# Kernel tuning notes

Measured on AMD Instinct MI355X. Metric: run time of the kernel, lower is better.

The kernel has to match this reference:

```python
import jax, jax.numpy as jnp
import numpy as np

H = 16       # num query heads
KV = 4       # num kv heads
D = 64       # head_dim
EPS = 1e-6


def setup_inputs() -> dict:
    key = jax.random.key(0)
    ks = jax.random.split(key, 12)
    B, N, E = 2, 2048, 1024
    s = 0.02
    return {
        "x": jax.random.normal(ks[0], (B, N, E), jnp.float32),
        "sin": jax.random.normal(ks[1], (N, D), jnp.float32),
        "cos": jax.random.normal(ks[2], (N, D), jnp.float32),
        "wq_w": jax.random.normal(ks[3], (E, E), jnp.float32) * s,
        "wq_b": jax.random.normal(ks[4], (E,), jnp.float32) * s,
        "wk_w": jax.random.normal(ks[5], (KV * D, E), jnp.float32) * s,
        "wk_b": jax.random.normal(ks[6], (KV * D,), jnp.float32) * s,
        "wv_w": jax.random.normal(ks[7], (KV * D, E), jnp.float32) * s,
        "wv_b": jax.random.normal(ks[8], (KV * D,), jnp.float32) * s,
        "qn_w": jnp.ones((D,), jnp.float32),
        "kn_w": jnp.ones((D,), jnp.float32),
        "proj_w": jax.random.normal(ks[9], (E, E), jnp.float32) * s,
        "proj_b": jax.random.normal(ks[10], (E,), jnp.float32) * s,
    }


def _rmsnorm(t, w):
    # t: [..., D]
    var = jnp.mean(t * t, axis=-1, keepdims=True)
    return t * jax.lax.rsqrt(var + EPS) * w


def _rope(t, sin, cos):
    # t: [B,h,N,D]; sin/cos: [N,D] broadcast
    x1, x2 = jnp.split(t, 2, axis=-1)
    rotated = jnp.concatenate([-x2, x1], axis=-1)
    return t * cos + rotated * sin


def reference(x, sin, cos, wq_w, wq_b, wk_w, wk_b, wv_w, wv_b,
              qn_w, kn_w, proj_w, proj_b):
    B, N, E = x.shape
    q = (x @ wq_w.T + wq_b).reshape(B, N, H, D).transpose(0, 2, 1, 3)   # [B,H,N,D]
    k = (x @ wk_w.T + wk_b).reshape(B, N, KV, D).transpose(0, 2, 1, 3)  # [B,KV,N,D]
    v = (x @ wv_w.T + wv_b).reshape(B, N, KV, D).transpose(0, 2, 1, 3)
    q = _rmsnorm(q, qn_w)
    k = _rmsnorm(k, kn_w)
    # GQA: repeat kv heads to match query heads (repeat_interleave on head dim)
    factor = H // KV
    k = jnp.repeat(k, factor, axis=1)  # [B,H,N,D]
    v = jnp.repeat(v, factor, axis=1)
    # RoPE (n_extra = 0 since sin covers full sequence)
    q = _rope(q, sin, cos)
    k = _rope(k, sin, cos)
    # scaled dot-product attention
    scale = 1.0 / np.sqrt(D).astype(np.float32)
    scores = jnp.einsum("bhqd,bhkd->bhqk", q, k) * scale
    attn = jax.nn.softmax(scores, axis=-1)
    out = jnp.einsum("bhqk,bhkd->bhqd", attn, v)      # [B,H,N,D]
    out = out.transpose(0, 2, 1, 3).reshape(B, N, E)  # [B,N,E]
    return out @ proj_w.T + proj_b
```

## Files before the change

### kernel.cpp

```cpp
#include <hip/hip_runtime.h>
#include <hip/hip_bf16.h>
#include <math.h>


#define N_SEQ 2048
#define EMB   1024
#define NH    16
#define NKV   4
#define HD    64
#define BATCH 2
#define M_TOT 4096
#define QKV_N 1536

typedef __attribute__((ext_vector_type(8)))  short short8;
typedef __attribute__((ext_vector_type(4)))  float f32x4;
typedef __attribute__((ext_vector_type(16))) float f32x16;

__device__ __forceinline__ ushort f2bf(float f) {
    union { __hip_bfloat16 h; ushort u; } cv;
    cv.h = __float2bfloat16(f);
    return cv.u;
}
__device__ __forceinline__ float bf2f(ushort u) {
    union { __hip_bfloat16 h; ushort u; } cv;
    cv.u = u;
    return __bfloat162float(cv.h);
}
__device__ __forceinline__ uint pack2bf(float a, float b) {
    union { __hip_bfloat162 h; uint u; } cv;
    cv.h = __float22bfloat162_rn(float2{a, b});
    return cv.u;
}

__device__ __forceinline__ void g2lds16(const ushort* g, ushort* l) {
    __builtin_amdgcn_global_load_lds(
        (const __attribute__((address_space(1))) unsigned int*)g,
        (__attribute__((address_space(3))) unsigned int*)l, 16, 0, 0);
}

__device__ __forceinline__ void cvt4(const float* __restrict__ s,
                                     ushort* __restrict__ d, long g, long gd) {
    const float4 v = ((const float4*)s)[g];
    ushort4 o;
    o.x = f2bf(v.x); o.y = f2bf(v.y); o.z = f2bf(v.z); o.w = f2bf(v.w);
    ((ushort4*)d)[gd] = o;
}

__global__ __launch_bounds__(256) void prep_kernel(
    const float* __restrict__ x,  const float* __restrict__ wq,
    const float* __restrict__ wk, const float* __restrict__ wv,
    const float* __restrict__ wp, const float* __restrict__ bq,
    const float* __restrict__ bk, const float* __restrict__ bv,
    ushort* __restrict__ xb, ushort* __restrict__ Wqkv,
    ushort* __restrict__ Wproj, float* __restrict__ bqkv)
{
    const long i = (long)blockIdx.x * 256 + threadIdx.x;
    if (i < 1048576) {
        cvt4(x, xb, i, i);
    } else if (i < 1310720) {
        const long g = i - 1048576;
        cvt4(wq, Wqkv, g, g);
    } else if (i < 1376256) {
        const long g = i - 1310720;
        cvt4(wk, Wqkv, g, 262144 + g);
    } else if (i < 1441792) {
        const long g = i - 1376256;
        cvt4(wv, Wqkv, g, 327680 + g);
    } else if (i < 1703936) {
        const long g = i - 1441792;
        cvt4(wp, Wproj, g, g);
    } else if (i < 1704320) {
        const long j = i - 1703936;
        float4 v;
        if (j < 256)      v = ((const float4*)bq)[j];
        else if (j < 320) v = ((const float4*)bk)[j - 256];
        else              v = ((const float4*)bv)[j - 320];
        ((float4*)bqkv)[j] = v;
    }
}

__global__ __launch_bounds__(256) void gemm_qkv_fused(
    const ushort* __restrict__ A, const ushort* __restrict__ W,
    const float* __restrict__ bias,
    const float* __restrict__ qn_w, const float* __restrict__ kn_w,
    const float* __restrict__ sinp, const float* __restrict__ cosp,
    ushort* __restrict__ Qb, ushort* __restrict__ Kf,
    ushort* __restrict__ Vf)
{
    __shared__ ushort SMEM[6144];
    ushort* As = SMEM;
    ushort* Bs = SMEM + 4096;

    const int tid = threadIdx.x;
    const int m0 = blockIdx.y * 128, n0 = blockIdx.x * 64;
    const int w = tid >> 6, lane = tid & 63;
    const int quad = lane >> 4, l16 = lane & 15;
    const int wm = w * 32;
    const int K = EMB;

    f32x4 acc[2][4] = {};

    float bb[4];
#pragma unroll
    for (int j = 0; j < 4; ++j) bb[j] = bias[n0 + j * 16 + l16];

    const int r0 = tid >> 2;
    const int c8 = (tid & 3) * 8;
    const ushort* Ap = A + (size_t)(m0 + r0) * K + c8;
    const ushort* Wp = W + (size_t)(n0 + r0) * K + c8;
    ushort* AsW = As + w * 512;
    ushort* BsW = Bs + w * 512;

    for (int k0 = 0; k0 < K; k0 += 32) {
        __syncthreads();
        g2lds16(Ap + k0, AsW);
        g2lds16(Ap + (size_t)64 * K + k0, AsW + 2048);
        g2lds16(Wp + k0, BsW);
        __syncthreads();

        short8 aF[2], bF[4];
#pragma unroll
        for (int i = 0; i < 2; ++i)
            aF[i] = *(const short8*)&As[(wm + i * 16 + l16) * 32 + quad * 8];
#pragma unroll
        for (int j = 0; j < 4; ++j)
            bF[j] = *(const short8*)&Bs[(j * 16 + l16) * 32 + quad * 8];
        __builtin_amdgcn_s_setprio(1);
#pragma unroll
        for (int i = 0; i < 2; ++i)
#pragma unroll
            for (int j = 0; j < 4; ++j)
                acc[i][j] = __builtin_amdgcn_mfma_f32_16x16x32_bf16(
                    aF[i], bF[j], acc[i][j], 0, 0, 0);
        __builtin_amdgcn_s_setprio(0);
    }

    if (n0 < 1280) {
        const bool isQ = (n0 < 1024);
        const float* nw = isQ ? qn_w : kn_w;
        const float oscale = isQ ? 0.125f : 1.0f;
        float nwv[4];
#pragma unroll
        for (int j = 0; j < 4; ++j) nwv[j] = nw[j * 16 + l16];

#pragma unroll
        for (int i = 0; i < 2; ++i) {
#pragma unroll
            for (int r = 0; r < 4; ++r) {
                const int m = m0 + wm + i * 16 + quad * 4 + r;
                const int n = m & (N_SEQ - 1);
                const int bI = m >> 11;

                float v4[4];
                float ssum = 0.0f;
#pragma unroll
                for (int j = 0; j < 4; ++j) {
                    v4[j] = acc[i][j][r] + bb[j];
                    ssum += v4[j] * v4[j];
                }
                ssum += __shfl_xor(ssum, 1, 64);
                ssum += __shfl_xor(ssum, 2, 64);
                ssum += __shfl_xor(ssum, 4, 64);
                ssum += __shfl_xor(ssum, 8, 64);
                const float rinv = rsqrtf(ssum * (1.0f / 64.0f) + 1e-6f);

                float tn[4], val[4];
#pragma unroll
                for (int j = 0; j < 4; ++j) tn[j] = v4[j] * rinv * nwv[j];
#pragma unroll
                for (int j = 0; j < 4; ++j) {
                    const int d = j * 16 + l16;
                    const float rot = (j < 2) ? -tn[j + 2] : tn[j - 2];
                    val[j] = (tn[j] * cosp[n * HD + d] + rot * sinp[n * HD + d]) * oscale;
                }

                if (isQ) {
                    const size_t qrow =
                        ((size_t)((bI << 4) + (n0 >> 6)) * N_SEQ + n) * HD;
#pragma unroll
                    for (int j = 0; j < 4; ++j)
                        Qb[qrow + j * 16 + l16] = f2bf(val[j]);
                } else {
                    const int kvh = (n0 >> 6) - 16;
                    const int kt = n >> 6, rr = n & 63;
                    const int ss2 = rr >> 5, l32k = rr & 31;
                    const size_t kb =
                        ((size_t)(bI * NKV + kvh) * 32 + kt) * 4096 + l32k * 16 + l16;
#pragma unroll
                    for (int j = 0; j < 4; ++j)
                        Kf[kb + (ss2 * 4 + j) * 512] = f2bf(val[j]);
                }
            }
        }
    } else {
        const int kvv = (n0 - 1280) >> 6;
        const int bI = m0 >> 11;
        const int kt0 = (m0 & (N_SEQ - 1)) >> 6;
        ushort* L = SMEM;

        const int c = tid >> 5;
        const int l32v = tid & 31;
        const int row0 = (c >> 2) * 32 + ((c >> 1) & 1) * 16;
        const int dcol = (c & 1) * 32 + l32v;

#pragma unroll
        for (int h = 0; h < 2; ++h) {
            __syncthreads();
            if ((w >> 1) == h) {
                const int kl0 = wm - h * 64;
#pragma unroll
                for (int i = 0; i < 2; ++i)
#pragma unroll
                    for (int r = 0; r < 4; ++r) {
                        const int kl = kl0 + i * 16 + quad * 4 + r;
#pragma unroll
                        for (int j = 0; j < 4; ++j)
                            L[kl * 68 + j * 16 + l16] = f2bf(acc[i][j][r] + bb[j]);
                    }
            }
            __syncthreads();
            short8 o0, o1;
#pragma unroll
            for (int e = 0; e < 8; ++e) o0[e] = (short)L[(row0 + e) * 68 + dcol];
#pragma unroll
            for (int e = 0; e < 8; ++e) o1[e] = (short)L[(row0 + 8 + e) * 68 + dcol];
            const size_t vb = ((size_t)(bI * NKV + kvv) * 32 + kt0 + h) * 4096
                              + c * 512 + l32v * 16;
            *(short8*)&Vf[vb] = o0;
            *(short8*)&Vf[vb + 8] = o1;
        }
    }
}

template <bool BF16OUT>
__global__ __launch_bounds__(256) void gemm_mfma_kernel(
    const ushort* __restrict__ A, const ushort* __restrict__ W,
    const float* __restrict__ bias, void* __restrict__ Cout,
    int K, int ldc)
{
    __shared__ ushort As[128 * 32];
    __shared__ ushort Bs[64 * 32];

    const int tid = threadIdx.x;
    const int m0 = blockIdx.y * 128, n0 = blockIdx.x * 64;
    const int w = tid >> 6, lane = tid & 63;
    const int quad = lane >> 4, l16 = lane & 15;
    const int wm = w * 32;

    f32x4 acc[2][4] = {};

    float bb[4];
#pragma unroll
    for (int j = 0; j < 4; ++j) bb[j] = bias[n0 + j * 16 + l16];

    const int r0 = tid >> 2;
    const int c8 = (tid & 3) * 8;
    const ushort* Ap = A + (size_t)(m0 + r0) * K + c8;
    const ushort* Wp = W + (size_t)(n0 + r0) * K + c8;
    ushort* AsW = As + w * 512;
    ushort* BsW = Bs + w * 512;

    for (int k0 = 0; k0 < K; k0 += 32) {
        __syncthreads();
        g2lds16(Ap + k0, AsW);
        g2lds16(Ap + (size_t)64 * K + k0, AsW + 2048);
        g2lds16(Wp + k0, BsW);
        __syncthreads();

        short8 aF[2], bF[4];
#pragma unroll
        for (int i = 0; i < 2; ++i)
            aF[i] = *(const short8*)&As[(wm + i * 16 + l16) * 32 + quad * 8];
#pragma unroll
        for (int j = 0; j < 4; ++j)
            bF[j] = *(const short8*)&Bs[(j * 16 + l16) * 32 + quad * 8];
        __builtin_amdgcn_s_setprio(1);
#pragma unroll
        for (int i = 0; i < 2; ++i)
#pragma unroll
            for (int j = 0; j < 4; ++j)
                acc[i][j] = __builtin_amdgcn_mfma_f32_16x16x32_bf16(
                    aF[i], bF[j], acc[i][j], 0, 0, 0);
        __builtin_amdgcn_s_setprio(0);
    }

#pragma unroll
    for (int i = 0; i < 2; ++i) {
        const int rowb = m0 + wm + i * 16 + quad * 4;
#pragma unroll
        for (int j = 0; j < 4; ++j) {
            const int col = n0 + j * 16 + l16;
#pragma unroll
            for (int r = 0; r < 4; ++r) {
                const float vv = acc[i][j][r] + bb[j];
                if (BF16OUT)
                    ((ushort*)Cout)[(size_t)(rowb + r) * ldc + col] = f2bf(vv);
                else
                    ((float*)Cout)[(size_t)(rowb + r) * ldc + col] = vv;
            }
        }
    }
}

__global__ __launch_bounds__(256, 4) void flash_mfma32_kernel(
    const ushort* __restrict__ Qb, const ushort* __restrict__ Kf,
    const ushort* __restrict__ Vf, ushort* __restrict__ Ob)
{
    __shared__ float fsm[4352];

    const int qt = blockIdx.x;
    const int bh = blockIdx.y;
    const int b = bh >> 4, h = bh & 15;
    const int kvh = h >> 2;
    const int tid = threadIdx.x;
    const int w = tid >> 6, lane = tid & 63;
    const int l32 = lane & 31, l5 = lane >> 5;
    const int qg = w & 1;
    const int kh = w >> 1;

    const ushort* Qg = Qb + ((size_t)bh * N_SEQ + qt * 64 + qg * 32) * HD;
    const size_t kvbase = (size_t)(b * NKV + kvh) * (32 * 4096);
    const ushort* Kp = Kf + kvbase;
    const ushort* Vp = Vf + kvbase;
    const int loff = l32 * 16 + l5 * 8;

    short8 qF[4];
#pragma unroll
    for (int c = 0; c < 4; ++c)
        qF[c] = *(const short8*)&Qg[(size_t)l32 * HD + c * 16 + l5 * 8];

    f32x16 Oa[2] = {};
    float mrow = -3.0e38f, lrow = 0.0f;

    for (int i = 0; i < 16; ++i) {
        const int kt = kh * 16 + i;
        const ushort* Kt = Kp + kt * 4096;
        const ushort* Vt = Vp + kt * 4096;

        short8 kT[2][4];
#pragma unroll
        for (int s = 0; s < 2; ++s)
#pragma unroll
            for (int c = 0; c < 4; ++c)
                kT[s][c] = *(const short8*)&Kt[(s * 4 + c) * 512 + loff];
        short8 vT[2][2][2];
#pragma unroll
        for (int s = 0; s < 2; ++s)
#pragma unroll
            for (int t = 0; t < 2; ++t)
#pragma unroll
                for (int d2 = 0; d2 < 2; ++d2)
                    vT[s][t][d2] = *(const short8*)&Vt[((s * 2 + t) * 2 + d2) * 512 + loff];

        f32x16 Sv[2] = {};
#pragma unroll
        for (int s = 0; s < 2; ++s)
#pragma unroll
            for (int c = 0; c < 4; ++c)
                Sv[s] = __builtin_amdgcn_mfma_f32_32x32x16_bf16(kT[s][c], qF[c], Sv[s], 0, 0, 0);

        float mx = -3.0e38f;
#pragma unroll
        for (int s = 0; s < 2; ++s)
#pragma unroll
            for (int r = 0; r < 16; ++r) mx = fmaxf(mx, Sv[s][r]);
        mx = fmaxf(mx, __shfl_xor(mx, 32, 64));
        const float mnew = fmaxf(mrow, mx);
        const float alpha = __expf(mrow - mnew);
        mrow = mnew;
        float rs = 0.0f;
#pragma unroll
        for (int s = 0; s < 2; ++s)
#pragma unroll
            for (int r = 0; r < 16; ++r) {
                Sv[s][r] = __expf(Sv[s][r] - mnew);
                rs += Sv[s][r];
            }
        rs += __shfl_xor(rs, 32, 64);
        lrow = lrow * alpha + rs;
#pragma unroll
        for (int t = 0; t < 2; ++t)
#pragma unroll
            for (int r = 0; r < 16; ++r) Oa[t][r] *= alpha;

        uint P2[2][8];
#pragma unroll
        for (int s = 0; s < 2; ++s)
#pragma unroll
            for (int g = 0; g < 4; ++g)
#pragma unroll
                for (int hh = 0; hh < 2; ++hh)
                    P2[s][g * 2 + hh] =
                        pack2bf(Sv[s][4 * g + 2 * hh], Sv[s][4 * g + 2 * hh + 1]);

#pragma unroll
        for (int s = 0; s < 2; ++s)
#pragma unroll
            for (int t = 0; t < 2; ++t) {
                const uint snd0 = l5 ? P2[s][4 * t + 0] : P2[s][4 * t + 2];
                const uint snd1 = l5 ? P2[s][4 * t + 1] : P2[s][4 * t + 3];
                const uint kp0  = l5 ? P2[s][4 * t + 2] : P2[s][4 * t + 0];
                const uint kp1  = l5 ? P2[s][4 * t + 3] : P2[s][4 * t + 1];
                const uint rcv0 = __shfl_xor(snd0, 32, 64);
                const uint rcv1 = __shfl_xor(snd1, 32, 64);
                union { uint u[4]; short8 s8; } pb;
                pb.u[0] = l5 ? rcv0 : kp0;
                pb.u[1] = l5 ? rcv1 : kp1;
                pb.u[2] = l5 ? kp0 : rcv0;
                pb.u[3] = l5 ? kp1 : rcv1;
#pragma unroll
                for (int d2 = 0; d2 < 2; ++d2)
                    Oa[d2] = __builtin_amdgcn_mfma_f32_32x32x16_bf16(
                        vT[s][t][d2], pb.s8, Oa[d2], 0, 0, 0);
            }
    }

    float* buf = fsm + qg * 2176;
    if (kh == 1) {
#pragma unroll
        for (int d2 = 0; d2 < 2; ++d2)
#pragma unroll
            for (int r = 0; r < 16; ++r)
                buf[(d2 * 16 + r) * 64 + lane] = Oa[d2][r];
        buf[2048 + lane] = mrow;
        buf[2112 + lane] = lrow;
    }
    __syncthreads();

    if (kh == 0) {
        const float mb = buf[2048 + lane];
        const float lb = buf[2112 + lane];
        const float M = fmaxf(mrow, mb);
        const float ea = __expf(mrow - M), eb = __expf(mb - M);
        lrow = lrow * ea + lb * eb;
#pragma unroll
        for (int d2 = 0; d2 < 2; ++d2)
#pragma unroll
            for (int r = 0; r < 16; ++r)
                Oa[d2][r] = Oa[d2][r] * ea + buf[(d2 * 16 + r) * 64 + lane] * eb;
    }
    __syncthreads();

    ushort* Os = (ushort*)fsm;
    if (kh == 0) {
        const float inv = 1.0f / lrow;
#pragma unroll
        for (int d2 = 0; d2 < 2; ++d2)
#pragma unroll
            for (int r = 0; r < 16; ++r) {
                const int d = d2 * 32 + (r & 3) + 8 * (r >> 2) + 4 * l5;
                Os[(qg * 32 + l32) * 68 + d] = f2bf(Oa[d2][r] * inv);
            }
    }
    __syncthreads();

    const int row = tid >> 2, cc = (tid & 3) * 16;
#pragma unroll
    for (int i = 0; i < 2; ++i) {
        const short8 v = *(const short8*)&Os[row * 68 + cc + i * 8];
        *(short8*)&Ob[((size_t)b * N_SEQ + qt * 64 + row) * EMB + h * HD + cc + i * 8] = v;
    }
}

extern "C" void kernel_launch(void* const* d_in, const int* in_sizes, int n_in,
                              void* d_out, int out_size, void* d_ws, size_t ws_size,
                              hipStream_t stream)
{
    const float* x      = (const float*)d_in[0];
    const float* sinp   = (const float*)d_in[1];
    const float* cosp   = (const float*)d_in[2];
    const float* wq_w   = (const float*)d_in[3];
    const float* wq_b   = (const float*)d_in[4];
    const float* wk_w   = (const float*)d_in[5];
    const float* wk_b   = (const float*)d_in[6];
    const float* wv_w   = (const float*)d_in[7];
    const float* wv_b   = (const float*)d_in[8];
    const float* qn_w   = (const float*)d_in[9];
    const float* kn_w   = (const float*)d_in[10];
    const float* proj_w = (const float*)d_in[11];
    const float* proj_b = (const float*)d_in[12];
    float* out = (float*)d_out;

    ushort* Tq    = (ushort*)d_ws;
    ushort* xb    = Tq + 6291456;
    ushort* Wqkv  = xb + 4194304;
    ushort* Wproj = Wqkv + 1572864;
    float*  bqkv  = (float*)(Wproj + 1048576);
    ushort* Qb    = (ushort*)(bqkv + 1536);
    ushort* Kf    = Qb + 4194304;
    ushort* Vf    = Kf + 1048576;

    prep_kernel<<<6658, 256, 0, stream>>>(x, wq_w, wk_w, wv_w, proj_w,
                                          wq_b, wk_b, wv_b,
                                          xb, Wqkv, Wproj, bqkv);

    gemm_qkv_fused<<<dim3(QKV_N / 64, M_TOT / 128), 256, 0, stream>>>(
        xb, Wqkv, bqkv, qn_w, kn_w, sinp, cosp, Qb, Kf, Vf);

    flash_mfma32_kernel<<<dim3(32, 32), 256, 0, stream>>>(Qb, Kf, Vf, xb);

    gemm_mfma_kernel<false><<<dim3(EMB / 64, M_TOT / 128), 256, 0, stream>>>(
        xb, Wproj, proj_b, out, EMB, EMB);
}
```

Baseline: 204.4 us.

## Double-buffer LDS tiles in QKV and projection GEMM main loops

Both bf16 MFMA GEMM kernels now hold two LDS buffers for the A and W tiles. The loop is restructured so the async global-to-LDS loads for the next K slice are issued before the MFMA work on the current slice, and the loop is unrolled by two. The goal is to hide global load latency behind matrix math instead of serialising load, barrier and compute each step. The cost is double the shared memory per block, which can reduce occupancy. The compiler may also insert conservative waitcnts on the in-flight LDS DMA that limit the overlap.

```diff
diff --git a/kernel.cpp b/kernel.cpp
--- a/kernel.cpp
+++ b/kernel.cpp
@@ -36,6 +36,36 @@
     __builtin_amdgcn_global_load_lds(
         (const __attribute__((address_space(1))) unsigned int*)g,
         (__attribute__((address_space(3))) unsigned int*)l, 16, 0, 0);
+}
+
+__device__ __forceinline__ void stage3(const ushort* Ap, const ushort* Wp,
+                                       int K, ushort* AsW, ushort* BsW, int kk)
+{
+    g2lds16(Ap + kk, AsW);
+    g2lds16(Ap + (size_t)64 * K + kk, AsW + 2048);
+    g2lds16(Wp + kk, BsW);
+}
+
+__device__ __forceinline__ void mfma_phase(const ushort* __restrict__ Asb,
+                                           const ushort* __restrict__ Bsb,
+                                           int wm, int l16, int quad,
+                                           f32x4 (&acc)[2][4])
+{
+    short8 aF[2], bF[4];
+#pragma unroll
+    for (int i = 0; i < 2; ++i)
+        aF[i] = *(const short8*)&Asb[(wm + i * 16 + l16) * 32 + quad * 8];
+#pragma unroll
+    for (int j = 0; j < 4; ++j)
+        bF[j] = *(const short8*)&Bsb[(j * 16 + l16) * 32 + quad * 8];
+    __builtin_amdgcn_s_setprio(1);
+#pragma unroll
+    for (int i = 0; i < 2; ++i)
+#pragma unroll
+        for (int j = 0; j < 4; ++j)
+            acc[i][j] = __builtin_amdgcn_mfma_f32_16x16x32_bf16(
+                aF[i], bF[j], acc[i][j], 0, 0, 0);
+    __builtin_amdgcn_s_setprio(0);
 }
 
 __device__ __forceinline__ void cvt4(const float* __restrict__ s,
@@ -87,9 +117,11 @@
     ushort* __restrict__ Qb, ushort* __restrict__ Kf,
     ushort* __restrict__ Vf)
 {
-    __shared__ ushort SMEM[6144];
-    ushort* As = SMEM;
-    ushort* Bs = SMEM + 4096;
+    __shared__ ushort SMEM[12288];
+    ushort* As0 = SMEM;
+    ushort* Bs0 = SMEM + 4096;
+    ushort* As1 = SMEM + 6144;
+    ushort* Bs1 = SMEM + 10240;
 
     const int tid = threadIdx.x;
     const int m0 = blockIdx.y * 128, n0 = blockIdx.x * 64;
@@ -108,31 +140,19 @@
     const int c8 = (tid & 3) * 8;
     const ushort* Ap = A + (size_t)(m0 + r0) * K + c8;
     const ushort* Wp = W + (size_t)(n0 + r0) * K + c8;
-    ushort* AsW = As + w * 512;
-    ushort* BsW = Bs + w * 512;
-
-    for (int k0 = 0; k0 < K; k0 += 32) {
+    ushort* As0W = As0 + w * 512;
+    ushort* Bs0W = Bs0 + w * 512;
+    ushort* As1W = As1 + w * 512;
+    ushort* Bs1W = Bs1 + w * 512;
+
+    stage3(Ap, Wp, K, As0W, Bs0W, 0);
+    for (int k0 = 0; k0 < K; k0 += 64) {
         __syncthreads();
-        g2lds16(Ap + k0, AsW);
-        g2lds16(Ap + (size_t)64 * K + k0, AsW + 2048);
-        g2lds16(Wp + k0, BsW);
+        stage3(Ap, Wp, K, As1W, Bs1W, k0 + 32);
+        mfma_phase(As0, Bs0, wm, l16, quad, acc);
         __syncthreads();
-
-        short8 aF[2], bF[4];
-#pragma unroll
-        for (int i = 0; i < 2; ++i)
-            aF[i] = *(const short8*)&As[(wm + i * 16 + l16) * 32 + quad * 8];
-#pragma unroll
-        for (int j = 0; j < 4; ++j)
-            bF[j] = *(const short8*)&Bs[(j * 16 + l16) * 32 + quad * 8];
-        __builtin_amdgcn_s_setprio(1);
-#pragma unroll
-        for (int i = 0; i < 2; ++i)
-#pragma unroll
-            for (int j = 0; j < 4; ++j)
-                acc[i][j] = __builtin_amdgcn_mfma_f32_16x16x32_bf16(
-                    aF[i], bF[j], acc[i][j], 0, 0, 0);
-        __builtin_amdgcn_s_setprio(0);
+        if (k0 + 64 < K) stage3(Ap, Wp, K, As0W, Bs0W, k0 + 64);
+        mfma_phase(As1, Bs1, wm, l16, quad, acc);
     }
 
     if (n0 < 1280) {
@@ -238,8 +258,11 @@
     const float* __restrict__ bias, void* __restrict__ Cout,
     int K, int ldc)
 {
-    __shared__ ushort As[128 * 32];
-    __shared__ ushort Bs[64 * 32];
+    __shared__ ushort SMEM[12288];
+    ushort* As0 = SMEM;
+    ushort* Bs0 = SMEM + 4096;
+    ushort* As1 = SMEM + 6144;
+    ushort* Bs1 = SMEM + 10240;
 
     const int tid = threadIdx.x;
     const int m0 = blockIdx.y * 128, n0 = blockIdx.x * 64;
@@ -257,31 +280,19 @@
     const int c8 = (tid & 3) * 8;
     const ushort* Ap = A + (size_t)(m0 + r0) * K + c8;
     const ushort* Wp = W + (size_t)(n0 + r0) * K + c8;
-    ushort* AsW = As + w * 512;
-    ushort* BsW = Bs + w * 512;
-
-    for (int k0 = 0; k0 < K; k0 += 32) {
+    ushort* As0W = As0 + w * 512;
+    ushort* Bs0W = Bs0 + w * 512;
+    ushort* As1W = As1 + w * 512;
+    ushort* Bs1W = Bs1 + w * 512;
+
+    stage3(Ap, Wp, K, As0W, Bs0W, 0);
+    for (int k0 = 0; k0 < K; k0 += 64) {
         __syncthreads();
-        g2lds16(Ap + k0, AsW);
-        g2lds16(Ap + (size_t)64 * K + k0, AsW + 2048);
-        g2lds16(Wp + k0, BsW);
+        stage3(Ap, Wp, K, As1W, Bs1W, k0 + 32);
+        mfma_phase(As0, Bs0, wm, l16, quad, acc);
         __syncthreads();
-
-        short8 aF[2], bF[4];
-#pragma unroll
-        for (int i = 0; i < 2; ++i)
-            aF[i] = *(const short8*)&As[(wm + i * 16 + l16) * 32 + quad * 8];
-#pragma unroll
-        for (int j = 0; j < 4; ++j)
-            bF[j] = *(const short8*)&Bs[(j * 16 + l16) * 32 + quad * 8];
-        __builtin_amdgcn_s_setprio(1);
-#pragma unroll
-        for (int i = 0; i < 2; ++i)
-#pragma unroll
-            for (int j = 0; j < 4; ++j)
-                acc[i][j] = __builtin_amdgcn_mfma_f32_16x16x32_bf16(
-                    aF[i], bF[j], acc[i][j], 0, 0, 0);
-        __builtin_amdgcn_s_setprio(0);
+        if (k0 + 64 < K) stage3(Ap, Wp, K, As0W, Bs0W, k0 + 64);
+        mfma_phase(As1, Bs1, wm, l16, quad, acc);
     }
 
 #pragma unroll
```

Result: faster. 199.2 us (-2.6%).
